# Kernel tuning notes

Measured on AMD Instinct MI355X. Metric: run time of the kernel, lower is better.

The kernel has to match this reference:

```python
import jax, jax.numpy as jnp
import numpy as np

INPUT, HIDDEN, OUTPUT = 512, 1024, 512
T, B = 512, 64
SIGMA = 0.01


def setup_inputs() -> dict:
    key = jax.random.key(0)
    k1, k2, k3, k4 = jax.random.split(key, 4)
    X = jax.random.normal(k1, (T, B, INPUT), dtype=jnp.float32)
    W_xh = jax.random.normal(k2, (INPUT, HIDDEN), dtype=jnp.float32) * SIGMA
    W_hh = jax.random.normal(k3, (HIDDEN, HIDDEN), dtype=jnp.float32) * SIGMA
    b_h = jnp.zeros((HIDDEN,), dtype=jnp.float32)
    W_hq = jax.random.normal(k4, (HIDDEN, OUTPUT), dtype=jnp.float32) * SIGMA
    b_q = jnp.zeros((OUTPUT,), dtype=jnp.float32)
    return {"X": X, "W_xh": W_xh, "W_hh": W_hh, "b_h": b_h, "W_hq": W_hq, "b_q": b_q}


def reference(X, W_xh, W_hh, b_h, W_hq, b_q):
    # Vanilla RNN: h_t = tanh(x_t @ W_xh + h_{t-1} @ W_hh + b_h); y_t = h_t @ W_hq + b_q
    # Precompute input projections for all timesteps in one big GEMM.
    Xproj = jnp.einsum('tbi,ih->tbh', X, W_xh) + b_h  # [T, B, H]
    h0 = jnp.zeros((X.shape[1], W_hh.shape[0]), dtype=X.dtype)

    def step(h, xp):
        h = jnp.tanh(xp + h @ W_hh)
        return h, h

    _, states = jax.lax.scan(step, h0, Xproj)  # states: [T, B, H]
    outputs = jnp.einsum('tbh,ho->tbo', states, W_hq) + b_q  # [T, B, O]
    return (outputs, states)
```

## Files before the change

kernel.cpp:

```cpp
#include <hip/hip_runtime.h>

typedef __attribute__((ext_vector_type(8))) short short8;
typedef __attribute__((ext_vector_type(4))) float f32x4;
typedef __attribute__((ext_vector_type(4))) int i32x4;
typedef unsigned long long u64;

__device__ __forceinline__ unsigned short f2bf(float f) {
  unsigned u = __builtin_bit_cast(unsigned, f);
  u += 0x7fffu + ((u >> 16) & 1u);
  return (unsigned short)(u >> 16);
}

__device__ __forceinline__ float fast_tanh(float x) {
  float e = __expf(2.0f * x);
  return 1.0f - __fdividef(2.0f, e + 1.0f);
}

__global__ __launch_bounds__(256) void gemm_bias(
    const float* __restrict__ A, const float* __restrict__ B,
    const float* __restrict__ bias, float* __restrict__ C,
    int M, int N, int K)
{
  __shared__ short a_lds[128 * 32];
  __shared__ short b_lds[32 * 128];
  const int tid = threadIdx.x;
  const int lane = tid & 63;
  const int w = tid >> 6;
  const int wm = w >> 1, wn = w & 1;
  const long m0 = (long)blockIdx.x * 128;
  const int n0 = blockIdx.y * 128;

  f32x4 acc[4][4];
#pragma unroll
  for (int i = 0; i < 4; ++i)
#pragma unroll
    for (int j = 0; j < 4; ++j) acc[i][j] = (f32x4){0.f, 0.f, 0.f, 0.f};

  for (int k0 = 0; k0 < K; k0 += 32) {
#pragma unroll
    for (int it = 0; it < 2; ++it) {
      int tsk = tid + (it << 8);
      int r = tsk >> 2;
      int kg = tsk & 3;
      const float* src = A + (m0 + r) * (long)K + (k0 + kg * 8);
      float4 f0 = *(const float4*)src;
      float4 f1 = *(const float4*)(src + 4);
      short8 v;
      v[0] = f2bf(f0.x); v[1] = f2bf(f0.y); v[2] = f2bf(f0.z); v[3] = f2bf(f0.w);
      v[4] = f2bf(f1.x); v[5] = f2bf(f1.y); v[6] = f2bf(f1.z); v[7] = f2bf(f1.w);
      *(short8*)&a_lds[(((r >> 4) * 64) + kg * 16 + (r & 15)) * 8] = v;
    }
#pragma unroll
    for (int rep = 0; rep < 2; ++rep) {
      int nl = tid & 127;
      int kg = (tid >> 7) + rep * 2;
      const float* src = B + (long)(k0 + kg * 8) * N + (n0 + nl);
      short8 v;
#pragma unroll
      for (int r2 = 0; r2 < 8; ++r2) v[r2] = f2bf(src[(long)r2 * N]);
      *(short8*)&b_lds[(((nl >> 4) * 64) + kg * 16 + (nl & 15)) * 8] = v;
    }
    __syncthreads();
    short8 af[4], bfr[4];
#pragma unroll
    for (int mt = 0; mt < 4; ++mt)
      af[mt] = *(const short8*)&a_lds[((wm * 4 + mt) * 64 + lane) * 8];
#pragma unroll
    for (int nt = 0; nt < 4; ++nt)
      bfr[nt] = *(const short8*)&b_lds[((wn * 4 + nt) * 64 + lane) * 8];
#pragma unroll
    for (int mt = 0; mt < 4; ++mt)
#pragma unroll
      for (int nt = 0; nt < 4; ++nt)
        acc[mt][nt] = __builtin_amdgcn_mfma_f32_16x16x32_bf16(
            af[mt], bfr[nt], acc[mt][nt], 0, 0, 0);
    __syncthreads();
  }
#pragma unroll
  for (int nt = 0; nt < 4; ++nt) {
    int col = n0 + wn * 64 + nt * 16 + (lane & 15);
    float bv = bias[col];
#pragma unroll
    for (int mt = 0; mt < 4; ++mt) {
      long row = m0 + wm * 64 + mt * 16 + ((lane >> 4) * 4);
#pragma unroll
      for (int r = 0; r < 4; ++r)
        C[(row + r) * (long)N + col] = acc[mt][nt][r] + bv;
    }
  }
}

__global__ __launch_bounds__(64, 1) void rnn_scan(
    const float* __restrict__ Whh, float* __restrict__ xs,
    unsigned short* __restrict__ hbuf, int* __restrict__ flags)
{
  __shared__ short wlds[32 * 2 * 64 * 8];
  const int H = 1024;
  const int lane = threadIdx.x;
  const int wg = blockIdx.x;
  const int rg = wg >> 5;
  const int cg = wg & 31;
  const int n0 = cg * 32;
  const int r0 = rg * 16;

  for (int p = 0; p < 32; ++p) {
#pragma unroll
    for (int mt = 0; mt < 2; ++mt) {
      const float* src = Whh + (long)(p * 32 + (lane >> 4) * 8) * H
                       + (n0 + mt * 16 + (lane & 15));
      short8 v;
#pragma unroll
      for (int j = 0; j < 8; ++j) v[j] = f2bf(src[(long)j * H]);
      *(short8*)&wlds[(((p * 2 + mt) * 64) + lane) * 8] = v;
    }
  }
  __syncthreads();

  const int m = lane & 15;
  const int q4 = (lane >> 4) * 4;
  const int chunk_rd = m * 32 + (lane >> 4) * 8;
  const int myflag = wg * 4;
  union Pack { unsigned short us[4]; u64 q; };

  for (int t = 0; t < 512; ++t) {
    const int slot_r = (t & 1) ^ 1;
    const int slot_w = t & 1;
    float* xrow = xs + (long)t * 64 * H;
    float* xbase = xrow + (long)(r0 + m) * H + n0 + q4;

    f32x4 xp0 = *(const f32x4*)xbase;
    f32x4 xp1 = *(const f32x4*)(xbase + 16);

    if (lane < 32) {
      const int* fp = flags + (rg * 32 + lane) * 4;
      while (__hip_atomic_load(fp, __ATOMIC_RELAXED, __HIP_MEMORY_SCOPE_AGENT) < t) {}
    }

    const unsigned short* hrd =
        hbuf + (size_t)slot_r * 65536 + (size_t)rg * 16384 + chunk_rd;
    i32x4 hraw[32];
#pragma unroll
    for (int p = 0; p < 32; ++p) {
      asm volatile("global_load_dwordx4 %0, %1, off sc0 sc1"
                   : "=v"(hraw[p]) : "v"(hrd + (size_t)p * 512) : "memory");
    }
    asm volatile("s_waitcnt vmcnt(0)" ::: "memory");
    __builtin_amdgcn_sched_barrier(0);

    f32x4 acc0 = {0.f, 0.f, 0.f, 0.f}, acc1 = {0.f, 0.f, 0.f, 0.f};
#pragma unroll
    for (int p = 0; p < 32; ++p) {
      short8 a0 = *(const short8*)&wlds[((p * 2 + 0) * 64 + lane) * 8];
      short8 a1 = *(const short8*)&wlds[((p * 2 + 1) * 64 + lane) * 8];
      short8 hb = __builtin_bit_cast(short8, hraw[p]);
      acc0 = __builtin_amdgcn_mfma_f32_16x16x32_bf16(a0, hb, acc0, 0, 0, 0);
      acc1 = __builtin_amdgcn_mfma_f32_16x16x32_bf16(a1, hb, acc1, 0, 0, 0);
    }

    float h0[4], h1[4];
    Pack pv0, pv1;
#pragma unroll
    for (int r = 0; r < 4; ++r) {
      h0[r] = fast_tanh(acc0[r] + xp0[r]);
      h1[r] = fast_tanh(acc1[r] + xp1[r]);
      pv0.us[r] = f2bf(h0[r]);
      pv1.us[r] = f2bf(h1[r]);
    }
    unsigned short* hwr = hbuf + (size_t)slot_w * 65536 + (size_t)wg * 512;
    __hip_atomic_store((u64*)(hwr + m * 32 + q4), pv0.q,
                       __ATOMIC_RELAXED, __HIP_MEMORY_SCOPE_AGENT);
    __hip_atomic_store((u64*)(hwr + m * 32 + 16 + q4), pv1.q,
                       __ATOMIC_RELAXED, __HIP_MEMORY_SCOPE_AGENT);
    asm volatile("s_waitcnt vmcnt(0)" ::: "memory");
    if (lane == 0)
      __hip_atomic_store(flags + myflag, t + 1,
                         __ATOMIC_RELAXED, __HIP_MEMORY_SCOPE_AGENT);

    *(f32x4*)xbase = (f32x4){h0[0], h0[1], h0[2], h0[3]};
    *(f32x4*)(xbase + 16) = (f32x4){h1[0], h1[1], h1[2], h1[3]};
  }
}

extern "C" void kernel_launch(void* const* d_in, const int* in_sizes, int n_in,
                              void* d_out, int out_size, void* d_ws, size_t ws_size,
                              hipStream_t stream)
{
  const float* X   = (const float*)d_in[0];
  const float* Wxh = (const float*)d_in[1];
  const float* Whh = (const float*)d_in[2];
  const float* bh  = (const float*)d_in[3];
  const float* Whq = (const float*)d_in[4];
  const float* bq  = (const float*)d_in[5];

  float* outputs = (float*)d_out;
  float* states  = outputs + (long)512 * 64 * 512;

  unsigned short* hbuf = (unsigned short*)d_ws;
  int* flags = (int*)((char*)d_ws + (size_t)2 * 64 * 1024 * 2);

  hipMemsetAsync(d_ws, 0, (size_t)2 * 64 * 1024 * 2 + 2048, stream);

  dim3 g1(32768 / 128, 1024 / 128);
  gemm_bias<<<g1, 256, 0, stream>>>(X, Wxh, bh, states, 32768, 1024, 512);

  rnn_scan<<<128, 64, 0, stream>>>(Whh, states, hbuf, flags);

  dim3 g3(32768 / 128, 512 / 128);
  gemm_bias<<<g3, 256, 0, stream>>>(states, Whq, bq, outputs, 32768, 512, 1024);
}
```

Baseline: 2.383 ms.

## Replace per-step flag polling with timestep-tagged hidden-state words in RNN scan

Adds a new scan kernel in which each 32-bit hidden-state pair is stored alongside its timestep tag in a 64-bit word, so consumers check data validity directly instead of waiting on a separate flag written after a store fence. This removes the store-waitcnt-flag round trip on the serial critical path of every timestep. Hidden-state loads are also software-pipelined eight slices deep, interleaved with MFMAs, with a retry when any tag mismatches. The cost is double the hidden-state traffic and a possible full recompute on a stale read; the old flag kernel is kept as a fallback when the workspace is too small.

Measured after the change: 3.020 ms. +26.7%, slower.

```diff
diff --git a/kernel.cpp b/kernel.cpp
--- a/kernel.cpp
+++ b/kernel.cpp
@@ -90,7 +90,141 @@
   }
 }
 
-__global__ __launch_bounds__(64, 1) void rnn_scan(
+
+#define RNN_LOAD(P) \
+    asm volatile("global_load_dwordx4 %0, %1, off sc0 sc1" \
+        : "=v"(braw[(P) & 7][0]) : "v"(hrd + (size_t)(P) * 2048) : "memory"); \
+    asm volatile("global_load_dwordx4 %0, %1, off sc0 sc1" \
+        : "=v"(braw[(P) & 7][1]) : "v"(hrd + (size_t)(P) * 2048 + 16) : "memory");
+
+#define RNN_STEP(P, WL) do { \
+    asm volatile("s_waitcnt " WL ::: "memory"); \
+    __builtin_amdgcn_sched_barrier(0); \
+    i32x4 p0 = braw[(P) & 7][0]; \
+    i32x4 p1 = braw[(P) & 7][1]; \
+    diff |= (unsigned)(p0.y ^ (int)exp_tag) | (unsigned)(p0.w ^ (int)exp_tag) \
+          | (unsigned)(p1.y ^ (int)exp_tag) | (unsigned)(p1.w ^ (int)exp_tag); \
+    i32x4 bi; bi.x = p0.x; bi.y = p0.z; bi.z = p1.x; bi.w = p1.z; \
+    short8 bfrag = __builtin_bit_cast(short8, bi); \
+    short8 a0 = *(const short8*)&wlds[(((P) * 2 + 0) * 64 + lane) * 8]; \
+    short8 a1 = *(const short8*)&wlds[(((P) * 2 + 1) * 64 + lane) * 8]; \
+    acc0 = __builtin_amdgcn_mfma_f32_16x16x32_bf16(a0, bfrag, acc0, 0, 0, 0); \
+    acc1 = __builtin_amdgcn_mfma_f32_16x16x32_bf16(a1, bfrag, acc1, 0, 0, 0); \
+    if ((P) + 8 < 32) { RNN_LOAD((P) + 8) } \
+  } while (0)
+
+__global__ __launch_bounds__(64, 1) void rnn_scan_tagged(
+    const float* __restrict__ Whh, float* __restrict__ xs,
+    char* __restrict__ hbuf)
+{
+  __shared__ short wlds[32 * 2 * 64 * 8];
+  const int H = 1024;
+  const int lane = threadIdx.x;
+  const int wg = blockIdx.x;
+  const int rg = wg >> 5;
+  const int cg = wg & 31;
+  const int n0 = cg * 32;
+  const int r0 = rg * 16;
+
+  for (int p = 0; p < 32; ++p) {
+#pragma unroll
+    for (int mt = 0; mt < 2; ++mt) {
+      const float* src = Whh + (long)(p * 32 + (lane >> 4) * 8) * H
+                       + (n0 + mt * 16 + (lane & 15));
+      short8 v;
+#pragma unroll
+      for (int j = 0; j < 8; ++j) v[j] = f2bf(src[(long)j * H]);
+      *(short8*)&wlds[(((p * 2 + mt) * 64) + lane) * 8] = v;
+    }
+  }
+  __syncthreads();
+
+  const int m = lane & 15;
+  const int kq = lane >> 4;
+  const int q4 = kq * 4;
+  const int q2 = kq * 2;
+
+  i32x4 braw[8][2];
+
+  for (int t = 0; t < 512; ++t) {
+    const int slot_r = (t & 1) ^ 1;
+    const int slot_w = t & 1;
+    char* ring_r = hbuf + (size_t)slot_r * 262144 + (size_t)rg * 65536;
+    char* ring_w = hbuf + (size_t)slot_w * 262144 + (size_t)rg * 65536;
+    const char* hrd = ring_r + m * 128 + kq * 32;
+
+    float* xrow = xs + (long)t * 64 * H;
+    float* xbase = xrow + (long)(r0 + m) * H + n0 + q4;
+    f32x4 xp0 = *(const f32x4*)xbase;
+    f32x4 xp1 = *(const f32x4*)(xbase + 16);
+
+    {
+      const u64* sp = (const u64*)(ring_r + (size_t)(lane & 31) * 2048);
+      const bool need = lane < 32;
+      while (true) {
+        bool ok = true;
+        if (need) {
+          u64 v = __hip_atomic_load(sp, __ATOMIC_RELAXED, __HIP_MEMORY_SCOPE_AGENT);
+          ok = ((unsigned)(v >> 32) >= (unsigned)t);
+        }
+        if (__all(ok)) break;
+      }
+    }
+    asm volatile("s_waitcnt vmcnt(0)" ::: "memory");
+    __builtin_amdgcn_sched_barrier(0);
+
+    const unsigned exp_tag = (unsigned)t;
+    f32x4 acc0, acc1;
+    unsigned diff;
+  retry:
+    acc0 = (f32x4){0.f, 0.f, 0.f, 0.f};
+    acc1 = (f32x4){0.f, 0.f, 0.f, 0.f};
+    diff = 0u;
+    RNN_LOAD(0) RNN_LOAD(1) RNN_LOAD(2) RNN_LOAD(3)
+    RNN_LOAD(4) RNN_LOAD(5) RNN_LOAD(6) RNN_LOAD(7)
+    RNN_STEP(0,  "vmcnt(14)"); RNN_STEP(1,  "vmcnt(14)"); RNN_STEP(2,  "vmcnt(14)");
+    RNN_STEP(3,  "vmcnt(14)"); RNN_STEP(4,  "vmcnt(14)"); RNN_STEP(5,  "vmcnt(14)");
+    RNN_STEP(6,  "vmcnt(14)"); RNN_STEP(7,  "vmcnt(14)"); RNN_STEP(8,  "vmcnt(14)");
+    RNN_STEP(9,  "vmcnt(14)"); RNN_STEP(10, "vmcnt(14)"); RNN_STEP(11, "vmcnt(14)");
+    RNN_STEP(12, "vmcnt(14)"); RNN_STEP(13, "vmcnt(14)"); RNN_STEP(14, "vmcnt(14)");
+    RNN_STEP(15, "vmcnt(14)"); RNN_STEP(16, "vmcnt(14)"); RNN_STEP(17, "vmcnt(14)");
+    RNN_STEP(18, "vmcnt(14)"); RNN_STEP(19, "vmcnt(14)"); RNN_STEP(20, "vmcnt(14)");
+    RNN_STEP(21, "vmcnt(14)"); RNN_STEP(22, "vmcnt(14)"); RNN_STEP(23, "vmcnt(14)");
+    RNN_STEP(24, "vmcnt(14)"); RNN_STEP(25, "vmcnt(12)"); RNN_STEP(26, "vmcnt(10)");
+    RNN_STEP(27, "vmcnt(8)");  RNN_STEP(28, "vmcnt(6)");  RNN_STEP(29, "vmcnt(4)");
+    RNN_STEP(30, "vmcnt(2)");  RNN_STEP(31, "vmcnt(0)");
+    if (__any((int)(diff != 0u))) goto retry;
+
+    float h0[4], h1[4];
+    unsigned short b0[4], b1[4];
+#pragma unroll
+    for (int r = 0; r < 4; ++r) {
+      h0[r] = fast_tanh(acc0[r] + xp0[r]);
+      h1[r] = fast_tanh(acc1[r] + xp1[r]);
+      b0[r] = f2bf(h0[r]);
+      b1[r] = f2bf(h1[r]);
+    }
+    const u64 tw = ((u64)(unsigned)(t + 1)) << 32;
+    char* hw = ring_w + (size_t)cg * 2048 + m * 128;
+    __hip_atomic_store((u64*)(hw + (q2 + 0) * 8),
+        (u64)((unsigned)b0[0] | ((unsigned)b0[1] << 16)) | tw,
+        __ATOMIC_RELAXED, __HIP_MEMORY_SCOPE_AGENT);
+    __hip_atomic_store((u64*)(hw + (q2 + 1) * 8),
+        (u64)((unsigned)b0[2] | ((unsigned)b0[3] << 16)) | tw,
+        __ATOMIC_RELAXED, __HIP_MEMORY_SCOPE_AGENT);
+    __hip_atomic_store((u64*)(hw + (q2 + 8) * 8),
+        (u64)((unsigned)b1[0] | ((unsigned)b1[1] << 16)) | tw,
+        __ATOMIC_RELAXED, __HIP_MEMORY_SCOPE_AGENT);
+    __hip_atomic_store((u64*)(hw + (q2 + 9) * 8),
+        (u64)((unsigned)b1[2] | ((unsigned)b1[3] << 16)) | tw,
+        __ATOMIC_RELAXED, __HIP_MEMORY_SCOPE_AGENT);
+
+    *(f32x4*)xbase = (f32x4){h0[0], h0[1], h0[2], h0[3]};
+    *(f32x4*)(xbase + 16) = (f32x4){h1[0], h1[1], h1[2], h1[3]};
+  }
+}
+
+__global__ __launch_bounds__(64, 1) void rnn_scan_flag(
     const float* __restrict__ Whh, float* __restrict__ xs,
     unsigned short* __restrict__ hbuf, int* __restrict__ flags)
 {
@@ -195,15 +329,18 @@
   float* outputs = (float*)d_out;
   float* states  = outputs + (long)512 * 64 * 512;
 
-  unsigned short* hbuf = (unsigned short*)d_ws;
-  int* flags = (int*)((char*)d_ws + (size_t)2 * 64 * 1024 * 2);
-
-  hipMemsetAsync(d_ws, 0, (size_t)2 * 64 * 1024 * 2 + 2048, stream);
-
   dim3 g1(32768 / 128, 1024 / 128);
   gemm_bias<<<g1, 256, 0, stream>>>(X, Wxh, bh, states, 32768, 1024, 512);
 
-  rnn_scan<<<128, 64, 0, stream>>>(Whh, states, hbuf, flags);
+  if (ws_size >= (size_t)524288) {
+    hipMemsetAsync(d_ws, 0, (size_t)524288, stream);
+    rnn_scan_tagged<<<128, 64, 0, stream>>>(Whh, states, (char*)d_ws);
+  } else {
+    unsigned short* hbuf = (unsigned short*)d_ws;
+    int* flags = (int*)((char*)d_ws + (size_t)2 * 64 * 1024 * 2);
+    hipMemsetAsync(d_ws, 0, (size_t)2 * 64 * 1024 * 2 + 2048, stream);
+    rnn_scan_flag<<<128, 64, 0, stream>>>(Whh, states, hbuf, flags);
+  }
 
   dim3 g3(32768 / 128, 512 / 128);
   gemm_bias<<<g3, 256, 0, stream>>>(states, Whq, bq, outputs, 32768, 512, 1024);
```
